# Performance work log

Measured on AMD Instinct MI355X. Metric: run time of the kernel, lower is better.

The kernel has to match this reference:

```python
import jax, jax.numpy as jnp
import numpy as np

N = 50000
EPS = 1e-5


def gcn_conv(x, W, b, src, dst, n):
    # x: [n, Cin]; W: [Cin, Cout]; src/dst: [E+n] with self-loops included
    h = x @ W  # dense GEMM
    deg = jax.ops.segment_sum(jnp.ones_like(dst, dtype=h.dtype), dst, num_segments=n)
    dinv = jnp.where(deg > 0, jax.lax.rsqrt(deg), 0.0)
    norm = dinv[src] * dinv[dst]  # [E+n]
    msgs = h[src] * norm[:, None]  # gather + scale
    out = jax.ops.segment_sum(msgs, dst, num_segments=n)  # scatter-add
    return out + b


def batch_norm(x, gamma, beta, mean, var):
    return (x - mean) * jax.lax.rsqrt(var + EPS) * gamma + beta


def setup_inputs() -> dict:
    key = jax.random.key(0)
    ks = jax.random.split(key, 16)
    IN, H, OUT, E = 1280, 256, 500, 1600000
    x = jax.random.normal(ks[0], (N, IN), dtype=jnp.float32)
    edge_index = jax.random.randint(ks[1], (2, E), 0, N, dtype=jnp.int64)
    def lin(k, cin, cout):
        return jax.random.normal(k, (cin, cout), dtype=jnp.float32) / np.sqrt(cin)
    return {
        "x": x,
        "edge_index": edge_index,
        "W1": lin(ks[2], IN, H), "b1": jnp.zeros((H,), jnp.float32),
        "g1": jnp.ones((H,), jnp.float32), "be1": jnp.zeros((H,), jnp.float32),
        "m1": 0.1 * jax.random.normal(ks[3], (H,), jnp.float32),
        "v1": 0.5 + jax.random.uniform(ks[4], (H,), jnp.float32),
        "W2": lin(ks[5], H, H), "b2": jnp.zeros((H,), jnp.float32),
        "g2": jnp.ones((H,), jnp.float32), "be2": jnp.zeros((H,), jnp.float32),
        "m2": 0.1 * jax.random.normal(ks[6], (H,), jnp.float32),
        "v2": 0.5 + jax.random.uniform(ks[7], (H,), jnp.float32),
        "W3": lin(ks[8], H, OUT), "b3": jnp.zeros((OUT,), jnp.float32),
    }


def reference(x, edge_index, W1, b1, g1, be1, m1, v1, W2, b2, g2, be2, m2, v2, W3, b3):
    n = x.shape[0]
    loops = jnp.arange(n, dtype=edge_index.dtype)
    src = jnp.concatenate([edge_index[0], loops])
    dst = jnp.concatenate([edge_index[1], loops])
    h = gcn_conv(x, W1, b1, src, dst, n)
    h = jax.nn.relu(batch_norm(h, g1, be1, m1, v1))
    h = gcn_conv(h, W2, b2, src, dst, n)
    h = jax.nn.relu(batch_norm(h, g2, be2, m2, v2))
    return gcn_conv(h, W3, b3, src, dst, n)
```

## Files before the change

kernel.cpp:

```cpp
#include <hip/hip_runtime.h>
#include <hip/hip_bf16.h>
#include <stdint.h>

typedef __attribute__((ext_vector_type(4))) float f32x4;
typedef __attribute__((ext_vector_type(8))) short s16x8;
typedef __attribute__((ext_vector_type(4))) unsigned short u16x4;

#define EPSBN 1e-5f

__device__ __forceinline__ float bf2f(unsigned short u) {
  union { unsigned int i; float f; } w; w.i = ((unsigned int)u) << 16; return w.f;
}
__device__ __forceinline__ unsigned short f2bf(float f) {
  __hip_bfloat16 h = __float2bfloat16(f);
  unsigned short u; __builtin_memcpy(&u, &h, 2); return u;
}
__device__ __forceinline__ void gld_lds16(const void* g, void* l) {
  __builtin_amdgcn_global_load_lds(
      (const __attribute__((address_space(1))) void*)(g),
      (__attribute__((address_space(3))) void*)(l), 16, 0, 0);
}

__global__ void k_count(const int* __restrict__ dst, unsigned* __restrict__ deg, int E) {
  int i = blockIdx.x * 256 + threadIdx.x;
  if (i < E) atomicAdd(&deg[dst[i]], 1u);
}
__global__ void k_prep2(const unsigned* __restrict__ deg, float* __restrict__ dinv,
                        unsigned* __restrict__ bsum, int n) {
  __shared__ unsigned s[256];
  int t = threadIdx.x, i = blockIdx.x * 256 + t;
  unsigned d = (i < n) ? deg[i] + 1u : 0u;
  if (i < n) dinv[i] = rsqrtf((float)d);
  s[t] = d;
  __syncthreads();
  for (int st = 128; st > 0; st >>= 1) {
    if (t < st) s[t] += s[t + st];
    __syncthreads();
  }
  if (t == 0) bsum[blockIdx.x] = s[0];
}
__global__ void k_scan_top(const unsigned* __restrict__ bsum, unsigned* __restrict__ bpre,
                           int nb, unsigned* __restrict__ offs, int n) {
  __shared__ unsigned s[256];
  int t = threadIdx.x;
  unsigned v = (t < nb) ? bsum[t] : 0u;
  s[t] = v; __syncthreads();
  for (int d = 1; d < 256; d <<= 1) {
    unsigned a = (t >= d) ? s[t - d] : 0u;
    __syncthreads();
    s[t] += a;
    __syncthreads();
  }
  bpre[t] = s[t] - v;
  if (t == 255) offs[n] = s[255];
}
__global__ void k_scan_fin(const unsigned* __restrict__ deg, const unsigned* __restrict__ bpre,
                           unsigned* __restrict__ offs, unsigned* __restrict__ cur, int n) {
  __shared__ unsigned s[256];
  int t = threadIdx.x, i = blockIdx.x * 256 + t;
  unsigned v = (i < n) ? deg[i] + 1u : 0u;
  s[t] = v; __syncthreads();
  for (int d = 1; d < 256; d <<= 1) {
    unsigned a = (t >= d) ? s[t - d] : 0u;
    __syncthreads();
    s[t] += a;
    __syncthreads();
  }
  if (i < n) {
    unsigned o = bpre[blockIdx.x] + s[t] - v;
    offs[i] = o; cur[i] = o;
  }
}
__global__ void k_fill(const int* __restrict__ src, const int* __restrict__ dst,
                       unsigned* __restrict__ cur, unsigned short* __restrict__ ewp,
                       int E, int n) {
  int i = blockIdx.x * 256 + threadIdx.x;
  int s, d;
  if (i < E)          { s = src[i]; d = dst[i]; }
  else if (i < E + n) { s = d = i - E; }
  else return;
  unsigned p = atomicAdd(&cur[d], 1u);
  ewp[p] = (unsigned short)s;
}
__global__ __launch_bounds__(256) void k_sortw(const unsigned* __restrict__ offs,
                                               unsigned short* __restrict__ ewp, int nN) {
  int wv = (blockIdx.x * 256 + threadIdx.x) >> 6;
  int lane = threadIdx.x & 63;
  if (wv >= nN) return;
  unsigned beg = offs[wv], end = offs[wv + 1];
  int len = (int)(end - beg);
  if (len > 64) return;
  int k = (lane < len) ? (int)ewp[beg + lane] : 0x10000;
#pragma unroll
  for (int size = 2; size <= 64; size <<= 1) {
#pragma unroll
    for (int stride = size >> 1; stride > 0; stride >>= 1) {
      int other = __shfl_xor(k, stride);
      bool up = (lane & size) == 0;
      bool lower = (lane & stride) == 0;
      k = (lower == up) ? min(k, other) : max(k, other);
    }
  }
  if (lane < len) ewp[beg + lane] = (unsigned short)k;
}
__global__ void k_wt3(const float* __restrict__ W1, unsigned short* __restrict__ Wt1,
                      const float* __restrict__ W2, unsigned short* __restrict__ Wt2,
                      const float* __restrict__ W3, unsigned short* __restrict__ Wt3,
                      unsigned short* __restrict__ bufA, unsigned short* __restrict__ bufB,
                      int nN) {
  const int n1 = 256 * 1280, n2 = 256 * 256, n3 = 512 * 256;
  int idx = blockIdx.x * 256 + threadIdx.x;
  if (idx >= n1 + n2 + n3) {
    int z = idx - (n1 + n2 + n3);
    if (z < 256)      bufA[(size_t)nN * 256 + z] = 0;
    else if (z < 512) bufB[(size_t)nN * 256 + (z - 256)] = 0;
    return;
  }
  const float* W; unsigned short* Wt; int K, N;
  if (idx < n1)           { W = W1; Wt = Wt1; K = 1280; N = 256; }
  else if (idx < n1 + n2) { W = W2; Wt = Wt2; K = 256;  N = 256; idx -= n1; }
  else                    { W = W3; Wt = Wt3; K = 256;  N = 500; idx -= n1 + n2; }
  int nn = idx / K, k = idx - nn * K;
  float v = (nn < N) ? W[(size_t)k * N + nn] : 0.f;
  Wt[idx] = f2bf(v);
}

#define BM 128
#define BK 64

template<int OUTMODE>
__global__ __launch_bounds__(256, 4) void k_gemm(
    const unsigned short* __restrict__ Au, const unsigned short* __restrict__ Bt,
    void* __restrict__ Coutv, const float* __restrict__ bias,
    const float* __restrict__ dinv, int M, int N, int K, int MT, int NT)
{
  __shared__ __align__(16) unsigned short As[BM * BK];
  __shared__ __align__(16) unsigned short Bs[128 * BK];

  int d = blockIdx.x;
  int xc = d & 7, sb = d >> 3;
  int nt = sb % NT, mt = (sb / NT) * 8 + xc;
  if (mt >= MT) return;
  int m0 = mt * BM, n0 = nt * 128;

  int tid = threadIdx.x, lane = tid & 63, wave = tid >> 6;
  int wm = wave >> 1, wn = wave & 1;
  int l15 = lane & 15, l4 = lane >> 4;

  f32x4 acc[4][4];
#pragma unroll
  for (int i = 0; i < 4; ++i)
#pragma unroll
    for (int j = 0; j < 4; ++j) acc[i][j] = 0.f;

  int srow[4], scg[4];
#pragma unroll
  for (int i = 0; i < 4; ++i) {
    int ci = (wave + 4 * i) * 64 + lane;
    srow[i] = ci >> 3;
    scg[i] = (ci & 7) ^ (srow[i] & 7);
  }

  int nk = K / BK;
  for (int kt = 0; kt < nk; ++kt) {
    __syncthreads();
#pragma unroll
    for (int i = 0; i < 4; ++i) {
      int gr = m0 + srow[i]; gr = gr < M ? gr : M - 1;
      gld_lds16(Au + (size_t)gr * K + kt * BK + scg[i] * 8, As + (wave + 4 * i) * 512);
    }
#pragma unroll
    for (int i = 0; i < 4; ++i) {
      int gn = n0 + srow[i];
      gld_lds16(Bt + (size_t)gn * K + kt * BK + scg[i] * 8, Bs + (wave + 4 * i) * 512);
    }
    __syncthreads();

#pragma unroll
    for (int ks = 0; ks < 2; ++ks) {
      s16x8 af[4], bf[4];
#pragma unroll
      for (int f = 0; f < 4; ++f) {
        int r = wm * 64 + f * 16 + l15;
        int ca = (ks * 4 + l4) ^ (r & 7);
        af[f] = *(const s16x8*)(As + r * 64 + ca * 8);
        int nloc = wn * 64 + f * 16 + l15;
        int cb = (ks * 4 + l4) ^ (nloc & 7);
        bf[f] = *(const s16x8*)(Bs + nloc * 64 + cb * 8);
      }
#pragma unroll
      for (int fm = 0; fm < 4; ++fm)
#pragma unroll
        for (int fn = 0; fn < 4; ++fn)
          acc[fm][fn] = __builtin_amdgcn_mfma_f32_16x16x32_bf16(af[fm], bf[fn], acc[fm][fn], 0, 0, 0);
    }
  }

#pragma unroll
  for (int fm = 0; fm < 4; ++fm) {
#pragma unroll
    for (int r = 0; r < 4; ++r) {
      int row = m0 + wm * 64 + fm * 16 + l4 * 4 + r;
      float dsc = (OUTMODE == 0 && row < M) ? dinv[row] : 0.f;
#pragma unroll
      for (int fn = 0; fn < 4; ++fn) {
        int col = n0 + wn * 64 + fn * 16 + l15;
        if (row < M && col < N) {
          if (OUTMODE == 1)
            ((float*)Coutv)[(size_t)row * N + col] = acc[fm][fn][r] + bias[col];
          else
            ((unsigned short*)Coutv)[(size_t)row * N + col] = f2bf(acc[fm][fn][r] * dsc);
        }
      }
    }
  }
}

__global__ __launch_bounds__(512, 4) void k_gemmF(
    const float* __restrict__ Af, const unsigned short* __restrict__ Bt,
    unsigned short* __restrict__ Cout, const float* __restrict__ dinv,
    int M, int N, int K)
{
  __shared__ __align__(16) float As[BM * BK];
  __shared__ __align__(16) unsigned short Bs[256 * BK];

  int mt = blockIdx.x;
  int m0 = mt * BM, n0 = 0;

  int tid = threadIdx.x, lane = tid & 63, wave = tid >> 6;
  int wm = wave >> 2, wn = wave & 3;
  int l15 = lane & 15, l4 = lane >> 4;

  f32x4 acc[4][4];
#pragma unroll
  for (int i = 0; i < 4; ++i)
#pragma unroll
    for (int j = 0; j < 4; ++j) acc[i][j] = 0.f;

  int arow[4], acs[4];
#pragma unroll
  for (int i = 0; i < 4; ++i) {
    int ci = i * 512 + tid;
    arow[i] = ci >> 4;
    int s = ((arow[i] & 7) << 1) | ((arow[i] >> 3) & 1);
    acs[i] = (ci & 15) ^ s;
  }
  int brow[4], bcg[4];
#pragma unroll
  for (int i = 0; i < 4; ++i) {
    int ci = i * 512 + tid;
    brow[i] = ci >> 3;
    bcg[i] = (ci & 7) ^ (brow[i] & 7);
  }

  int nk = K / BK;
  for (int kt = 0; kt < nk; ++kt) {
    __syncthreads();
#pragma unroll
    for (int i = 0; i < 4; ++i) {
      int gr = m0 + arow[i]; gr = gr < M ? gr : M - 1;
      gld_lds16(Af + (size_t)gr * K + kt * BK + acs[i] * 4,
                As + (size_t)(i * 512 + wave * 64) * 4);
    }
#pragma unroll
    for (int i = 0; i < 4; ++i) {
      int gn = n0 + brow[i];
      gld_lds16(Bt + (size_t)gn * K + kt * BK + bcg[i] * 8,
                Bs + (size_t)(i * 512 + wave * 64) * 8);
    }
    __syncthreads();

#pragma unroll
    for (int ks = 0; ks < 2; ++ks) {
      s16x8 af[4], bf[4];
#pragma unroll
      for (int f = 0; f < 4; ++f) {
        int r = wm * 64 + f * 16 + l15;
        int s = ((r & 7) << 1) | ((r >> 3) & 1);
        int gc0 = ks * 8 + 2 * l4;
        f32x4 a0 = *(const f32x4*)(As + r * 64 + (gc0 ^ s) * 4);
        f32x4 a1 = *(const f32x4*)(As + r * 64 + ((gc0 + 1) ^ s) * 4);
        s16x8 pk;
        pk[0] = (short)f2bf(a0[0]); pk[1] = (short)f2bf(a0[1]);
        pk[2] = (short)f2bf(a0[2]); pk[3] = (short)f2bf(a0[3]);
        pk[4] = (short)f2bf(a1[0]); pk[5] = (short)f2bf(a1[1]);
        pk[6] = (short)f2bf(a1[2]); pk[7] = (short)f2bf(a1[3]);
        af[f] = pk;
        int nloc = wn * 64 + f * 16 + l15;
        int cb = (ks * 4 + l4) ^ (nloc & 7);
        bf[f] = *(const s16x8*)(Bs + nloc * 64 + cb * 8);
      }
#pragma unroll
      for (int fm = 0; fm < 4; ++fm)
#pragma unroll
        for (int fn = 0; fn < 4; ++fn)
          acc[fm][fn] = __builtin_amdgcn_mfma_f32_16x16x32_bf16(af[fm], bf[fn], acc[fm][fn], 0, 0, 0);
    }
  }

#pragma unroll
  for (int fm = 0; fm < 4; ++fm) {
#pragma unroll
    for (int r = 0; r < 4; ++r) {
      int row = m0 + wm * 64 + fm * 16 + l4 * 4 + r;
      float dsc = (row < M) ? dinv[row] : 0.f;
#pragma unroll
      for (int fn = 0; fn < 4; ++fn) {
        int col = n0 + wn * 64 + fn * 16 + l15;
        if (row < M && col < N)
          Cout[(size_t)row * N + col] = f2bf(acc[fm][fn][r] * dsc);
      }
    }
  }
}

template<int BNRELU, int SCALEOUT>
__global__ __launch_bounds__(256) void k_agg(
    const unsigned short* __restrict__ h, const unsigned short* __restrict__ ewp,
    const unsigned* __restrict__ offs, const float* __restrict__ dinv,
    const float* __restrict__ bias, const float* __restrict__ gam,
    const float* __restrict__ bet, const float* __restrict__ mea,
    const float* __restrict__ var, unsigned short* __restrict__ outp, int nN)
{
  int wave = threadIdx.x >> 6, lane = threadIdx.x & 63;
  int v = blockIdx.x * 4 + wave;
  if (v >= nN) return;
  unsigned beg = offs[v], end = offs[v + 1];
  int len = (int)(end - beg);
  float dv = dinv[v];
  const unsigned short* hb = h + lane * 4;
  float a0 = 0, a1 = 0, a2 = 0, a3 = 0;

  for (int base = 0; base < len; base += 64) {
    int m = min(64, len - base);
    int myp = (lane < m) ? (int)ewp[beg + base + lane] : nN;
    int ng = (m + 15) >> 4;

    u16x4 q[16];
#pragma unroll
    for (int r = 0; r < 16; ++r) {
      int s = __shfl(myp, r);
      q[r] = *(const u16x4*)(hb + (size_t)s * 256);
    }
    for (int g = 1; g < ng; ++g) {
      u16x4 q2[16];
#pragma unroll
      for (int r = 0; r < 16; ++r) {
        int s = __shfl(myp, g * 16 + r);
        q2[r] = *(const u16x4*)(hb + (size_t)s * 256);
      }
#pragma unroll
      for (int r = 0; r < 16; ++r) {
        a0 += bf2f(q[r][0]); a1 += bf2f(q[r][1]);
        a2 += bf2f(q[r][2]); a3 += bf2f(q[r][3]);
      }
#pragma unroll
      for (int r = 0; r < 16; ++r) q[r] = q2[r];
    }
#pragma unroll
    for (int r = 0; r < 16; ++r) {
      a0 += bf2f(q[r][0]); a1 += bf2f(q[r][1]);
      a2 += bf2f(q[r][2]); a3 += bf2f(q[r][3]);
    }
  }

  float va[4] = {a0, a1, a2, a3};
  int ch0 = lane * 4;
#pragma unroll
  for (int j = 0; j < 4; ++j) {
    int ch = ch0 + j;
    float val = va[j] * dv;
    if (BNRELU) {
      val += bias[ch];
      val = (val - mea[ch]) * rsqrtf(var[ch] + EPSBN) * gam[ch] + bet[ch];
      val = fmaxf(val, 0.f);
    }
    if (SCALEOUT) val *= dv;
    outp[(size_t)v * 256 + ch] = f2bf(val);
  }
}

extern "C" void kernel_launch(void* const* d_in, const int* in_sizes, int n_in,
                              void* d_out, int out_size, void* d_ws, size_t ws_size,
                              hipStream_t stream) {
  const float* x   = (const float*)d_in[0];
  const int*   ei  = (const int*)d_in[1];
  const float* W1  = (const float*)d_in[2];
  const float* b1  = (const float*)d_in[3];
  const float* g1  = (const float*)d_in[4];
  const float* be1 = (const float*)d_in[5];
  const float* m1  = (const float*)d_in[6];
  const float* v1  = (const float*)d_in[7];
  const float* W2  = (const float*)d_in[8];
  const float* b2  = (const float*)d_in[9];
  const float* g2  = (const float*)d_in[10];
  const float* be2 = (const float*)d_in[11];
  const float* m2  = (const float*)d_in[12];
  const float* v2  = (const float*)d_in[13];
  const float* W3  = (const float*)d_in[14];
  const float* b3  = (const float*)d_in[15];

  const int IN = 1280, H = 256, OUT = 500, OUTP = 512;
  int E  = in_sizes[1] / 2;
  int nN = in_sizes[0] / IN;
  const int* srcI = ei;
  const int* dstI = ei + E;

  char* p = (char*)d_ws;
  auto carve = [&](size_t bytes) { char* r = p; p += (bytes + 511) & ~(size_t)511; return r; };
  unsigned short* Wt1 = (unsigned short*)carve((size_t)H * IN * 2);
  unsigned short* Wt2 = (unsigned short*)carve((size_t)H * H * 2);
  unsigned short* Wt3 = (unsigned short*)carve((size_t)OUTP * H * 2);
  unsigned* deg  = (unsigned*)carve((size_t)nN * 4);
  float*    dinv = (float*)carve((size_t)nN * 4);
  unsigned* offs = (unsigned*)carve((size_t)(nN + 1) * 4);
  unsigned* cur  = (unsigned*)carve((size_t)nN * 4);
  unsigned* bsum = (unsigned*)carve(256 * 4);
  unsigned* bpre = (unsigned*)carve(256 * 4);
  unsigned short* ewp = (unsigned short*)carve((size_t)(E + nN) * 2);
  unsigned short* bufA = (unsigned short*)carve((size_t)(nN + 1) * H * 2);
  unsigned short* bufB = (unsigned short*)carve((size_t)(nN + 1) * H * 2);

  hipMemsetAsync(deg, 0, (size_t)nN * 4, stream);

  int NB = (nN + 255) / 256;
  k_count<<<(E + 255) / 256, 256, 0, stream>>>(dstI, deg, E);
  k_prep2<<<NB, 256, 0, stream>>>(deg, dinv, bsum, nN);
  k_scan_top<<<1, 256, 0, stream>>>(bsum, bpre, NB, offs, nN);
  k_scan_fin<<<NB, 256, 0, stream>>>(deg, bpre, offs, cur, nN);
  k_fill<<<(E + nN + 255) / 256, 256, 0, stream>>>(srcI, dstI, cur, ewp, E, nN);
  k_sortw<<<(nN + 3) / 4, 256, 0, stream>>>(offs, ewp, nN);
  k_wt3<<<(256 * 1280 + 256 * 256 + 512 * 256 + 512 + 255) / 256, 256, 0, stream>>>(
      W1, Wt1, W2, Wt2, W3, Wt3, bufA, bufB, nN);

  int MT = (nN + BM - 1) / BM;
  int mg = (MT + 7) / 8;
  int nAgg = (nN + 3) / 4;

  k_gemmF<<<MT, 512, 0, stream>>>(x, Wt1, bufA, dinv, nN, H, IN);
  k_agg<1, 0><<<nAgg, 256, 0, stream>>>(bufA, ewp, offs, dinv, b1, g1, be1, m1, v1, bufB, nN);
  k_gemm<0><<<mg * 8 * 2, 256, 0, stream>>>(bufB, Wt2, bufA, nullptr, dinv, nN, H, H, MT, 2);
  k_agg<1, 1><<<nAgg, 256, 0, stream>>>(bufA, ewp, offs, dinv, b2, g2, be2, m2, v2, bufB, nN);
  k_agg<0, 0><<<nAgg, 256, 0, stream>>>(bufB, ewp, offs, dinv, nullptr, nullptr, nullptr,
                                        nullptr, nullptr, bufA, nN);
  k_gemm<1><<<mg * 8 * 4, 256, 0, stream>>>(bufA, Wt3, d_out, b3, nullptr, nN, OUT, H, MT, 4);
}
```

Measured before the change: 687.9 us.

## Double-buffer LDS tiles in fp32-input GEMM with smaller K step

The first-layer GEMM kernel that reads fp32 activations now uses two LDS buffers with a K tile of 32 instead of 64. Loads for the next K tile are issued before the MFMA work on the current tile, so the loop needs one barrier per iteration instead of two. This is meant to hide global-to-LDS latency behind compute, at the cost of more loop iterations and new swizzle patterns for the halved row width.

```diff
diff --git a/kernel.cpp b/kernel.cpp
--- a/kernel.cpp
+++ b/kernel.cpp
@@ -216,16 +216,20 @@
   }
 }
 
+#define FBK 32
+#define ASZ (BM * FBK)
+#define BSZ (256 * FBK)
+
 __global__ __launch_bounds__(512, 4) void k_gemmF(
     const float* __restrict__ Af, const unsigned short* __restrict__ Bt,
     unsigned short* __restrict__ Cout, const float* __restrict__ dinv,
     int M, int N, int K)
 {
-  __shared__ __align__(16) float As[BM * BK];
-  __shared__ __align__(16) unsigned short Bs[256 * BK];
+  __shared__ __align__(16) float As[2 * ASZ];
+  __shared__ __align__(16) unsigned short Bs[2 * BSZ];
 
   int mt = blockIdx.x;
-  int m0 = mt * BM, n0 = 0;
+  int m0 = mt * BM;
 
   int tid = threadIdx.x, lane = tid & 63, wave = tid >> 6;
   int wm = wave >> 2, wn = wave & 3;
@@ -237,65 +241,77 @@
 #pragma unroll
     for (int j = 0; j < 4; ++j) acc[i][j] = 0.f;
 
-  int arow[4], acs[4];
-#pragma unroll
-  for (int i = 0; i < 4; ++i) {
+  int arow[2], acs[2];
+#pragma unroll
+  for (int i = 0; i < 2; ++i) {
     int ci = i * 512 + tid;
-    arow[i] = ci >> 4;
-    int s = ((arow[i] & 7) << 1) | ((arow[i] >> 3) & 1);
-    acs[i] = (ci & 15) ^ s;
-  }
-  int brow[4], bcg[4];
-#pragma unroll
-  for (int i = 0; i < 4; ++i) {
+    arow[i] = ci >> 3;
+    acs[i] = (ci & 7) ^ (arow[i] & 7);
+  }
+  int brow[2], bcs[2];
+#pragma unroll
+  for (int i = 0; i < 2; ++i) {
     int ci = i * 512 + tid;
-    brow[i] = ci >> 3;
-    bcg[i] = (ci & 7) ^ (brow[i] & 7);
-  }
-
-  int nk = K / BK;
+    brow[i] = ci >> 2;
+    bcs[i] = (ci & 3) ^ ((brow[i] >> 1) & 3);
+  }
+  int gra[2];
+#pragma unroll
+  for (int i = 0; i < 2; ++i) {
+    int gr = m0 + arow[i]; gra[i] = gr < M ? gr : M - 1;
+  }
+
+  int nk = K / FBK;
+  int cur = 0;
+
+#pragma unroll
+  for (int i = 0; i < 2; ++i)
+    gld_lds16(Af + (size_t)gra[i] * K + acs[i] * 4, As + (size_t)(i * 512 + wave * 64) * 4);
+#pragma unroll
+  for (int i = 0; i < 2; ++i)
+    gld_lds16(Bt + (size_t)brow[i] * K + bcs[i] * 8, Bs + (size_t)(i * 512 + wave * 64) * 8);
+  __syncthreads();
+
   for (int kt = 0; kt < nk; ++kt) {
-    __syncthreads();
-#pragma unroll
-    for (int i = 0; i < 4; ++i) {
-      int gr = m0 + arow[i]; gr = gr < M ? gr : M - 1;
-      gld_lds16(Af + (size_t)gr * K + kt * BK + acs[i] * 4,
-                As + (size_t)(i * 512 + wave * 64) * 4);
-    }
-#pragma unroll
-    for (int i = 0; i < 4; ++i) {
-      int gn = n0 + brow[i];
-      gld_lds16(Bt + (size_t)gn * K + kt * BK + bcg[i] * 8,
-                Bs + (size_t)(i * 512 + wave * 64) * 8);
-    }
-    __syncthreads();
-
-#pragma unroll
-    for (int ks = 0; ks < 2; ++ks) {
-      s16x8 af[4], bf[4];
-#pragma unroll
-      for (int f = 0; f < 4; ++f) {
-        int r = wm * 64 + f * 16 + l15;
-        int s = ((r & 7) << 1) | ((r >> 3) & 1);
-        int gc0 = ks * 8 + 2 * l4;
-        f32x4 a0 = *(const f32x4*)(As + r * 64 + (gc0 ^ s) * 4);
-        f32x4 a1 = *(const f32x4*)(As + r * 64 + ((gc0 + 1) ^ s) * 4);
-        s16x8 pk;
-        pk[0] = (short)f2bf(a0[0]); pk[1] = (short)f2bf(a0[1]);
-        pk[2] = (short)f2bf(a0[2]); pk[3] = (short)f2bf(a0[3]);
-        pk[4] = (short)f2bf(a1[0]); pk[5] = (short)f2bf(a1[1]);
-        pk[6] = (short)f2bf(a1[2]); pk[7] = (short)f2bf(a1[3]);
-        af[f] = pk;
-        int nloc = wn * 64 + f * 16 + l15;
-        int cb = (ks * 4 + l4) ^ (nloc & 7);
-        bf[f] = *(const s16x8*)(Bs + nloc * 64 + cb * 8);
-      }
-#pragma unroll
-      for (int fm = 0; fm < 4; ++fm)
-#pragma unroll
-        for (int fn = 0; fn < 4; ++fn)
-          acc[fm][fn] = __builtin_amdgcn_mfma_f32_16x16x32_bf16(af[fm], bf[fn], acc[fm][fn], 0, 0, 0);
-    }
+    if (kt + 1 < nk) {
+      int nxt = cur ^ 1;
+      int kb = (kt + 1) * FBK;
+#pragma unroll
+      for (int i = 0; i < 2; ++i)
+        gld_lds16(Af + (size_t)gra[i] * K + kb + acs[i] * 4,
+                  As + (size_t)nxt * ASZ + (size_t)(i * 512 + wave * 64) * 4);
+#pragma unroll
+      for (int i = 0; i < 2; ++i)
+        gld_lds16(Bt + (size_t)brow[i] * K + kb + bcs[i] * 8,
+                  Bs + (size_t)nxt * BSZ + (size_t)(i * 512 + wave * 64) * 8);
+    }
+    const float* Ab = As + (size_t)cur * ASZ;
+    const unsigned short* Bb = Bs + (size_t)cur * BSZ;
+    s16x8 af[4], bf[4];
+#pragma unroll
+    for (int f = 0; f < 4; ++f) {
+      int r = wm * 64 + f * 16 + l15;
+      int sA = r & 7;
+      int g0 = 2 * l4;
+      f32x4 a0 = *(const f32x4*)(Ab + r * 32 + (g0 ^ sA) * 4);
+      f32x4 a1 = *(const f32x4*)(Ab + r * 32 + ((g0 + 1) ^ sA) * 4);
+      s16x8 pk;
+      pk[0] = (short)f2bf(a0[0]); pk[1] = (short)f2bf(a0[1]);
+      pk[2] = (short)f2bf(a0[2]); pk[3] = (short)f2bf(a0[3]);
+      pk[4] = (short)f2bf(a1[0]); pk[5] = (short)f2bf(a1[1]);
+      pk[6] = (short)f2bf(a1[2]); pk[7] = (short)f2bf(a1[3]);
+      af[f] = pk;
+      int nloc = wn * 64 + f * 16 + l15;
+      int cb = l4 ^ ((nloc >> 1) & 3);
+      bf[f] = *(const s16x8*)(Bb + nloc * 32 + cb * 8);
+    }
+#pragma unroll
+    for (int fm = 0; fm < 4; ++fm)
+#pragma unroll
+      for (int fn = 0; fn < 4; ++fn)
+        acc[fm][fn] = __builtin_amdgcn_mfma_f32_16x16x32_bf16(af[fm], bf[fn], acc[fm][fn], 0, 0, 0);
+    __syncthreads();
+    cur ^= 1;
   }
 
 #pragma unroll
@@ -306,7 +322,7 @@
       float dsc = (row < M) ? dinv[row] : 0.f;
 #pragma unroll
       for (int fn = 0; fn < 4; ++fn) {
-        int col = n0 + wn * 64 + fn * 16 + l15;
+        int col = wn * 64 + fn * 16 + l15;
         if (row < M && col < N)
           Cout[(size_t)row * N + col] = f2bf(acc[fm][fn][r] * dsc);
       }
```

Measured after the change: 682.8 us. About the same (-0.7%).
